# Kernel optimization log

Hardware: AMD Instinct MI355X
Metric: run time of the kernel (lower is better)

The kernel has to match this reference:

```python
import jax, jax.numpy as jnp
import numpy as np

B, S, H, I, E, K = 2, 2048, 1024, 2816, 8, 2


def setup_inputs() -> dict:
    key = jax.random.key(0)
    k1, k2, k3, k4, k5 = jax.random.split(key, 5)
    std = 0.02
    x = jax.random.normal(k1, (B, S, H), dtype=jnp.float32)
    gate_w = jax.random.normal(k2, (H, E), dtype=jnp.float32) * std   # router Linear(H,E), no bias
    Wg = jax.random.normal(k3, (E, H, I), dtype=jnp.float32) * std    # per-expert gate_proj
    Wu = jax.random.normal(k4, (E, H, I), dtype=jnp.float32) * std    # per-expert up_proj
    Wd = jax.random.normal(k5, (E, I, H), dtype=jnp.float32) * std    # per-expert down_proj
    return {"x": x, "gate_w": gate_w, "Wg": Wg, "Wu": Wu, "Wd": Wd}


def reference(x, gate_w, Wg, Wu, Wd):
    b, s, h = x.shape
    e = gate_w.shape[1]
    # --- Gating ---
    logits = jnp.einsum('bsh,he->bse', x, gate_w)                      # [B,S,E]
    top_vals, top_idx = jax.lax.top_k(logits, K)                       # [B,S,K]
    sel = (top_idx[..., None] == jnp.arange(e)).any(axis=-2)           # [B,S,E] bool, top-k mask
    sparse_logits = jnp.where(sel, logits, -jnp.inf)
    sparse_probs = jax.nn.softmax(sparse_logits, axis=-1)              # zero weight off top-k
    # --- Experts (dense over E, weighted by sparse probs; math identical to gather/scatter loop) ---
    xf = x.reshape(-1, h)                                              # [T,H], T=B*S
    g = jnp.einsum('th,ehi->tei', xf, Wg)                              # [T,E,I]
    u = jnp.einsum('th,ehi->tei', xf, Wu)
    act = jax.nn.silu(g) * u                                           # SwiGLU
    expert_out = jnp.einsum('tei,eih->teh', act, Wd)                   # [T,E,H]
    out = jnp.einsum('teh,te->th', expert_out, sparse_probs.reshape(-1, e))
    final_outputs = out.reshape(b, s, h)
    gate_logit = logits.reshape(-1, e)                                 # [B*S,E]
    return final_outputs, gate_logit
```

## Files before the change

kernel.cpp:

```cpp
#include <hip/hip_runtime.h>


namespace {
constexpr int TOKS = 4096;
constexpr int HDIM = 1024;
constexpr int IDIM = 2816;
constexpr int NEXP = 8;
constexpr int NROW = 8192;

constexpr size_t WGT_OFF = 0;
constexpr size_t WUT_OFF = 46137344;
constexpr size_t WDT_OFF = 92274688;
constexpr size_t A_OFF   = 138412032;
constexpr size_t ACT_OFF = 155189248;
constexpr size_t CNT_OFF = 201326592;
constexpr size_t OFS_OFF = CNT_OFF + 64;
constexpr size_t CUR_OFF = CNT_OFF + 128;
constexpr size_t TIX_OFF = CNT_OFF + 1024;
constexpr size_t TPR_OFF = TIX_OFF + 32768;
constexpr size_t SLT_OFF = TPR_OFF + 32768;
constexpr size_t PRT_OFF = 0;
}

typedef __attribute__((ext_vector_type(8))) short short8;
typedef __attribute__((ext_vector_type(8))) unsigned short ushort8;
typedef __attribute__((ext_vector_type(4))) float f32x4;

__device__ __forceinline__ unsigned short f2bf(float f) {
  union { float f; unsigned int u; } v; v.f = f;
  unsigned int u = v.u;
  return (unsigned short)((u + 0x7fffu + ((u >> 16) & 1u)) >> 16);
}

__device__ __forceinline__ void gl2lds16(const void* g, void* l) {
  __builtin_amdgcn_global_load_lds(
      (const __attribute__((address_space(1))) void*)g,
      (__attribute__((address_space(3))) void*)l, 16, 0, 0);
}

__global__ void k_init(int* __restrict__ cnt) {
  if (threadIdx.x < NEXP) cnt[threadIdx.x] = 0;
}

__global__ __launch_bounds__(256) void k_transpose(
    const float* __restrict__ in, unsigned short* __restrict__ out,
    int R, int C) {
  const size_t eoff = (size_t)blockIdx.z * R * C;
  in += eoff; out += eoff;
  __shared__ float tile[64][65];
  const int c0 = blockIdx.x * 64, r0 = blockIdx.y * 64;
  const int tid = threadIdx.x;
  const int rr = tid >> 4, cc4 = (tid & 15) * 4;
#pragma unroll
  for (int i = 0; i < 4; ++i) {
    int r = rr + i * 16;
    float4 v = *(const float4*)(in + (size_t)(r0 + r) * C + c0 + cc4);
    tile[r][cc4 + 0] = v.x; tile[r][cc4 + 1] = v.y;
    tile[r][cc4 + 2] = v.z; tile[r][cc4 + 3] = v.w;
  }
  __syncthreads();
  const int j = tid & 7;
#pragma unroll
  for (int i = 0; i < 2; ++i) {
    int c = (tid >> 3) + i * 32;
    ushort8 o;
#pragma unroll
    for (int k = 0; k < 8; ++k) o[k] = f2bf(tile[j * 8 + k][c]);
    *(ushort8*)(out + (size_t)(c0 + c) * R + r0 + j * 8) = o;
  }
}

__global__ __launch_bounds__(256) void k_gating(
    const float* __restrict__ x, const float* __restrict__ gw,
    float* __restrict__ logits_out, int* __restrict__ cnt,
    int2* __restrict__ tidx, float2* __restrict__ tprb) {
  const int lane = threadIdx.x & 63;
  const int t = blockIdx.x * 4 + (threadIdx.x >> 6);
  const float* xr = x + (size_t)t * HDIM;
  double acc[8];
#pragma unroll
  for (int e = 0; e < 8; ++e) acc[e] = 0.0;
#pragma unroll
  for (int j = 0; j < 16; ++j) {
    int h = lane + j * 64;
    float xv = xr[h];
    const float4* g = (const float4*)(gw + (size_t)h * 8);
    float4 g0 = g[0], g1 = g[1];
    acc[0] += (double)xv * g0.x; acc[1] += (double)xv * g0.y;
    acc[2] += (double)xv * g0.z; acc[3] += (double)xv * g0.w;
    acc[4] += (double)xv * g1.x; acc[5] += (double)xv * g1.y;
    acc[6] += (double)xv * g1.z; acc[7] += (double)xv * g1.w;
  }
#pragma unroll
  for (int off = 32; off > 0; off >>= 1) {
#pragma unroll
    for (int e = 0; e < 8; ++e) acc[e] += __shfl_down(acc[e], off);
  }
  if (lane == 0) {
    float lg[8];
#pragma unroll
    for (int e = 0; e < 8; ++e) lg[e] = (float)acc[e];
#pragma unroll
    for (int e = 0; e < 8; ++e) logits_out[(size_t)t * 8 + e] = lg[e];
    float v0 = lg[0]; int i0 = 0; float v1 = -3.0e38f; int i1 = 0;
#pragma unroll
    for (int e = 1; e < 8; ++e) {
      if (lg[e] > v0) { v1 = v0; i1 = i0; v0 = lg[e]; i0 = e; }
      else if (lg[e] > v1) { v1 = lg[e]; i1 = e; }
    }
    float ex = expf(v1 - v0);
    float p0 = 1.0f / (1.0f + ex);
    float p1 = ex / (1.0f + ex);
    tidx[t] = make_int2(i0, i1);
    tprb[t] = make_float2(p0, p1);
    atomicAdd(&cnt[i0], 1);
    atomicAdd(&cnt[i1], 1);
  }
}

__global__ void k_prefix(const int* __restrict__ cnt, int* __restrict__ offs,
                         int* __restrict__ cur) {
  if (threadIdx.x == 0) {
    int s = 0;
    for (int e = 0; e < NEXP; ++e) { offs[e] = s; cur[e] = s; s += cnt[e]; }
  }
}

__global__ __launch_bounds__(256) void k_build(
    const float* __restrict__ x, const int2* __restrict__ tidx,
    int* __restrict__ cur, int* __restrict__ slot_row,
    unsigned short* __restrict__ A) {
  const int t = blockIdx.x;
  __shared__ int rs[2];
  if (threadIdx.x == 0) {
    int2 ii = tidx[t];
    int r0 = atomicAdd(&cur[ii.x], 1);
    int r1 = atomicAdd(&cur[ii.y], 1);
    rs[0] = r0; rs[1] = r1;
    slot_row[t * 2] = r0; slot_row[t * 2 + 1] = r1;
  }
  __syncthreads();
  const int r0 = rs[0], r1 = rs[1];
  float4 v = ((const float4*)(x + (size_t)t * HDIM))[threadIdx.x];
  ushort4 b;
  b.x = f2bf(v.x); b.y = f2bf(v.y); b.z = f2bf(v.z); b.w = f2bf(v.w);
  ((ushort4*)(A + (size_t)r0 * HDIM))[threadIdx.x] = b;
  ((ushort4*)(A + (size_t)r1 * HDIM))[threadIdx.x] = b;
}

__global__ __launch_bounds__(256, 2) void k_gemm1(
    const unsigned short* __restrict__ A, const unsigned short* __restrict__ WgT,
    const unsigned short* __restrict__ WuT, unsigned short* __restrict__ act,
    const int* __restrict__ cnt, const int* __restrict__ offs) {
  const int e = blockIdx.z;
  const int ne = cnt[e];
  const int m0 = blockIdx.y * 128;
  if (m0 >= ne) return;
  const int off = offs[e];
  const int n0 = blockIdx.x * 64;
  const unsigned short* Bg = WgT + ((size_t)e * IDIM + n0) * HDIM;
  const unsigned short* Bu = WuT + ((size_t)e * IDIM + n0) * HDIM;

  __shared__ unsigned short As[128 * 64];
  __shared__ unsigned short Bgs[64 * 64];
  __shared__ unsigned short Bus[64 * 64];

  const int tid = threadIdx.x, w = tid >> 6, lane = tid & 63;
  const int lrow8 = lane >> 3;
  const int swz = ((lane & 7) ^ lrow8) * 8;
  const int m16 = lane & 15, quad = lane >> 4, l7 = lane & 7;

  f32x4 accg[2][4], accu[2][4];
#pragma unroll
  for (int mi = 0; mi < 2; ++mi)
#pragma unroll
    for (int ni = 0; ni < 4; ++ni) {
      accg[mi][ni] = (f32x4){0.f, 0.f, 0.f, 0.f};
      accu[mi][ni] = (f32x4){0.f, 0.f, 0.f, 0.f};
    }

  for (int kt = 0; kt < HDIM / 64; ++kt) {
    const int k0 = kt * 64;
#pragma unroll
    for (int i = 0; i < 4; ++i) {
      int gr = off + m0 + w * 32 + i * 8 + lrow8;
      gr = gr > (NROW - 1) ? (NROW - 1) : gr;
      gl2lds16(A + (size_t)gr * HDIM + k0 + swz, &As[(w * 32 + i * 8) * 64]);
    }
#pragma unroll
    for (int i = 0; i < 2; ++i) {
      int rl = w * 16 + i * 8 + lrow8;
      gl2lds16(Bg + (size_t)rl * HDIM + k0 + swz, &Bgs[(w * 16 + i * 8) * 64]);
      gl2lds16(Bu + (size_t)rl * HDIM + k0 + swz, &Bus[(w * 16 + i * 8) * 64]);
    }
    __syncthreads();
#pragma unroll
    for (int kk = 0; kk < 2; ++kk) {
      const int jc = ((kk * 4 + quad) ^ l7) * 8;
      short8 af[2], bgf[4], buf[4];
#pragma unroll
      for (int mi = 0; mi < 2; ++mi)
        af[mi] = *(const short8*)&As[(w * 32 + mi * 16 + m16) * 64 + jc];
#pragma unroll
      for (int ni = 0; ni < 4; ++ni) {
        bgf[ni] = *(const short8*)&Bgs[(ni * 16 + m16) * 64 + jc];
        buf[ni] = *(const short8*)&Bus[(ni * 16 + m16) * 64 + jc];
      }
#pragma unroll
      for (int mi = 0; mi < 2; ++mi)
#pragma unroll
        for (int ni = 0; ni < 4; ++ni) {
          accg[mi][ni] = __builtin_amdgcn_mfma_f32_16x16x32_bf16(
              af[mi], bgf[ni], accg[mi][ni], 0, 0, 0);
          accu[mi][ni] = __builtin_amdgcn_mfma_f32_16x16x32_bf16(
              af[mi], buf[ni], accu[mi][ni], 0, 0, 0);
        }
    }
    __syncthreads();
  }
#pragma unroll
  for (int mi = 0; mi < 2; ++mi)
#pragma unroll
    for (int ni = 0; ni < 4; ++ni)
#pragma unroll
      for (int r = 0; r < 4; ++r) {
        int ml = w * 32 + mi * 16 + quad * 4 + r;
        float g = accg[mi][ni][r];
        float u = accu[mi][ni][r];
        float s = g / (1.0f + __expf(-g));
        As[ml * 64 + ni * 16 + m16] = f2bf(s * u);
      }
  __syncthreads();
#pragma unroll
  for (int i = 0; i < 4; ++i) {
    int chunk = i * 256 + tid;
    int row = chunk >> 3, j = chunk & 7;
    if (m0 + row < ne)
      *(ushort8*)&act[(size_t)(off + m0 + row) * IDIM + n0 + j * 8] =
          *(const ushort8*)&As[row * 64 + j * 8];
  }
}

__global__ __launch_bounds__(256, 2) void k_gemm2(
    const unsigned short* __restrict__ act, const unsigned short* __restrict__ WdT,
    float* __restrict__ partial, const int* __restrict__ cnt,
    const int* __restrict__ offs) {
  const int e = blockIdx.z;
  const int ne = cnt[e];
  const int m0 = blockIdx.y * 128;
  if (m0 >= ne) return;
  const int off = offs[e];
  const int n0 = blockIdx.x * 128;
  const unsigned short* B = WdT + ((size_t)e * HDIM + n0) * IDIM;

  __shared__ unsigned short As[128 * 64];
  __shared__ unsigned short Bs[128 * 64];

  const int tid = threadIdx.x, w = tid >> 6, lane = tid & 63;
  const int lrow8 = lane >> 3;
  const int swz = ((lane & 7) ^ lrow8) * 8;
  const int m16 = lane & 15, quad = lane >> 4, l7 = lane & 7;
  const int wm = (w >> 1) * 64, wn = (w & 1) * 64;

  f32x4 acc[4][4];
#pragma unroll
  for (int mi = 0; mi < 4; ++mi)
#pragma unroll
    for (int ni = 0; ni < 4; ++ni) acc[mi][ni] = (f32x4){0.f, 0.f, 0.f, 0.f};

  for (int kt = 0; kt < IDIM / 64; ++kt) {
    const int k0 = kt * 64;
#pragma unroll
    for (int i = 0; i < 4; ++i) {
      int rl = w * 32 + i * 8 + lrow8;
      int gr = off + m0 + rl;
      gr = gr > (NROW - 1) ? (NROW - 1) : gr;
      gl2lds16(act + (size_t)gr * IDIM + k0 + swz, &As[(w * 32 + i * 8) * 64]);
      gl2lds16(B + (size_t)rl * IDIM + k0 + swz, &Bs[(w * 32 + i * 8) * 64]);
    }
    __syncthreads();
#pragma unroll
    for (int kk = 0; kk < 2; ++kk) {
      const int jc = ((kk * 4 + quad) ^ l7) * 8;
      short8 af[4], bf[4];
#pragma unroll
      for (int mi = 0; mi < 4; ++mi)
        af[mi] = *(const short8*)&As[(wm + mi * 16 + m16) * 64 + jc];
#pragma unroll
      for (int ni = 0; ni < 4; ++ni)
        bf[ni] = *(const short8*)&Bs[(wn + ni * 16 + m16) * 64 + jc];
#pragma unroll
      for (int mi = 0; mi < 4; ++mi)
#pragma unroll
        for (int ni = 0; ni < 4; ++ni)
          acc[mi][ni] = __builtin_amdgcn_mfma_f32_16x16x32_bf16(
              af[mi], bf[ni], acc[mi][ni], 0, 0, 0);
    }
    __syncthreads();
  }
#pragma unroll
  for (int mi = 0; mi < 4; ++mi)
#pragma unroll
    for (int ni = 0; ni < 4; ++ni)
#pragma unroll
      for (int r = 0; r < 4; ++r) {
        int ml = wm + mi * 16 + quad * 4 + r;
        if (m0 + ml < ne)
          partial[(size_t)(off + m0 + ml) * HDIM + n0 + wn + ni * 16 + m16] =
              acc[mi][ni][r];
      }
}

__global__ __launch_bounds__(256) void k_combine(
    const float* __restrict__ partial, const int* __restrict__ slot_row,
    const float2* __restrict__ tprb, float* __restrict__ out) {
  const int t = blockIdx.x;
  const int r0 = slot_row[2 * t], r1 = slot_row[2 * t + 1];
  const float2 p = tprb[t];
  float4 a = ((const float4*)(partial + (size_t)r0 * HDIM))[threadIdx.x];
  float4 b = ((const float4*)(partial + (size_t)r1 * HDIM))[threadIdx.x];
  float4 o;
  o.x = p.x * a.x + p.y * b.x;
  o.y = p.x * a.y + p.y * b.y;
  o.z = p.x * a.z + p.y * b.z;
  o.w = p.x * a.w + p.y * b.w;
  ((float4*)(out + (size_t)t * HDIM))[threadIdx.x] = o;
}

extern "C" void kernel_launch(void* const* d_in, const int* in_sizes, int n_in,
                              void* d_out, int out_size, void* d_ws, size_t ws_size,
                              hipStream_t stream) {
  const float* x  = (const float*)d_in[0];
  const float* gw = (const float*)d_in[1];
  const float* Wg = (const float*)d_in[2];
  const float* Wu = (const float*)d_in[3];
  const float* Wd = (const float*)d_in[4];
  float* out = (float*)d_out;
  char* ws = (char*)d_ws;

  unsigned short* WgT = (unsigned short*)(ws + WGT_OFF);
  unsigned short* WuT = (unsigned short*)(ws + WUT_OFF);
  unsigned short* WdT = (unsigned short*)(ws + WDT_OFF);
  unsigned short* A   = (unsigned short*)(ws + A_OFF);
  unsigned short* act = (unsigned short*)(ws + ACT_OFF);
  float* partial = (float*)(ws + PRT_OFF);
  int* cnt  = (int*)(ws + CNT_OFF);
  int* offs = (int*)(ws + OFS_OFF);
  int* cur  = (int*)(ws + CUR_OFF);
  int2* tidx = (int2*)(ws + TIX_OFF);
  float2* tprb = (float2*)(ws + TPR_OFF);
  int* slot_row = (int*)(ws + SLT_OFF);

  float* logits_out = out + (size_t)TOKS * HDIM;

  k_init<<<1, 64, 0, stream>>>(cnt);
  k_transpose<<<dim3(IDIM / 64, HDIM / 64, NEXP), 256, 0, stream>>>(Wg, WgT, HDIM, IDIM);
  k_transpose<<<dim3(IDIM / 64, HDIM / 64, NEXP), 256, 0, stream>>>(Wu, WuT, HDIM, IDIM);
  k_transpose<<<dim3(HDIM / 64, IDIM / 64, NEXP), 256, 0, stream>>>(Wd, WdT, IDIM, HDIM);
  k_gating<<<TOKS / 4, 256, 0, stream>>>(x, gw, logits_out, cnt, tidx, tprb);
  k_prefix<<<1, 64, 0, stream>>>(cnt, offs, cur);
  k_build<<<TOKS, 256, 0, stream>>>(x, tidx, cur, slot_row, A);
  k_gemm1<<<dim3(IDIM / 64, TOKS / 128, NEXP), 256, 0, stream>>>(A, WgT, WuT, act, cnt, offs);
  k_gemm2<<<dim3(HDIM / 128, TOKS / 128, NEXP), 256, 0, stream>>>(act, WdT, partial, cnt, offs);
  k_combine<<<TOKS, 256, 0, stream>>>(partial, slot_row, tprb, out);
}
```

Before: 710.0 us.

## Compact MoE tile list, merge transposes, and fold slot assignment into gating

Builds a compact list of (expert, row-tile) pairs in the prefix kernel so the grouped GEMMs launch only about 72 row tiles instead of 8x32 mostly-empty blocks. The three weight transposes and the counter init are merged into one launch, and per-expert slot ranks are taken from the gating atomics, which removes the second atomic pass in the build kernel. Gating also loads x with float4. This cuts launch count and wasted blocks that exit immediately, but adds a serial tile-list loop on one thread and makes the row order depend on atomic ordering.

```diff
diff --git a/kernel.cpp b/kernel.cpp
--- a/kernel.cpp
+++ b/kernel.cpp
@@ -15,10 +15,10 @@
 constexpr size_t ACT_OFF = 155189248;
 constexpr size_t CNT_OFF = 201326592;
 constexpr size_t OFS_OFF = CNT_OFF + 64;
-constexpr size_t CUR_OFF = CNT_OFF + 128;
+constexpr size_t TLN_OFF = CNT_OFF + 128;
+constexpr size_t TLS_OFF = CNT_OFF + 256;
 constexpr size_t TIX_OFF = CNT_OFF + 1024;
-constexpr size_t TPR_OFF = TIX_OFF + 32768;
-constexpr size_t SLT_OFF = TPR_OFF + 32768;
+constexpr size_t TPR_OFF = CNT_OFF + 66560;
 constexpr size_t PRT_OFF = 0;
 }
 
@@ -38,17 +38,22 @@
       (__attribute__((address_space(3))) void*)l, 16, 0, 0);
 }
 
-__global__ void k_init(int* __restrict__ cnt) {
-  if (threadIdx.x < NEXP) cnt[threadIdx.x] = 0;
-}
-
-__global__ __launch_bounds__(256) void k_transpose(
-    const float* __restrict__ in, unsigned short* __restrict__ out,
-    int R, int C) {
-  const size_t eoff = (size_t)blockIdx.z * R * C;
+__global__ __launch_bounds__(256) void k_transpose_all(
+    const float* __restrict__ Wg, const float* __restrict__ Wu,
+    const float* __restrict__ Wd, unsigned short* __restrict__ WgT,
+    unsigned short* __restrict__ WuT, unsigned short* __restrict__ WdT,
+    int* __restrict__ cnt) {
+  const int z = blockIdx.z;
+  if (z == 0 && blockIdx.x == 0 && threadIdx.x < NEXP) cnt[threadIdx.x] = 0;
+  const float* in; unsigned short* out; int C, R;
+  if (z < 8)       { in = Wg; out = WgT; C = IDIM; R = HDIM; }
+  else if (z < 16) { in = Wu; out = WuT; C = IDIM; R = HDIM; }
+  else             { in = Wd; out = WdT; C = HDIM; R = IDIM; }
+  const size_t eoff = (size_t)(z & 7) * HDIM * IDIM;
   in += eoff; out += eoff;
+  const int nbx = C / 64;
+  const int c0 = (blockIdx.x % nbx) * 64, r0 = (blockIdx.x / nbx) * 64;
   __shared__ float tile[64][65];
-  const int c0 = blockIdx.x * 64, r0 = blockIdx.y * 64;
   const int tid = threadIdx.x;
   const int rr = tid >> 4, cc4 = (tid & 15) * 4;
 #pragma unroll
@@ -73,23 +78,27 @@
 __global__ __launch_bounds__(256) void k_gating(
     const float* __restrict__ x, const float* __restrict__ gw,
     float* __restrict__ logits_out, int* __restrict__ cnt,
-    int2* __restrict__ tidx, float2* __restrict__ tprb) {
+    int4* __restrict__ tidx, float2* __restrict__ tprb) {
   const int lane = threadIdx.x & 63;
   const int t = blockIdx.x * 4 + (threadIdx.x >> 6);
-  const float* xr = x + (size_t)t * HDIM;
+  const float4* xr = (const float4*)(x + (size_t)t * HDIM);
   double acc[8];
 #pragma unroll
   for (int e = 0; e < 8; ++e) acc[e] = 0.0;
 #pragma unroll
-  for (int j = 0; j < 16; ++j) {
-    int h = lane + j * 64;
-    float xv = xr[h];
-    const float4* g = (const float4*)(gw + (size_t)h * 8);
-    float4 g0 = g[0], g1 = g[1];
-    acc[0] += (double)xv * g0.x; acc[1] += (double)xv * g0.y;
-    acc[2] += (double)xv * g0.z; acc[3] += (double)xv * g0.w;
-    acc[4] += (double)xv * g1.x; acc[5] += (double)xv * g1.y;
-    acc[6] += (double)xv * g1.z; acc[7] += (double)xv * g1.w;
+  for (int jj = 0; jj < 4; ++jj) {
+    float4 xv = xr[lane + jj * 64];
+    const int hb = (lane + jj * 64) * 4;
+    const float xs[4] = {xv.x, xv.y, xv.z, xv.w};
+#pragma unroll
+    for (int c = 0; c < 4; ++c) {
+      const float4* g = (const float4*)(gw + (size_t)(hb + c) * 8);
+      float4 g0 = g[0], g1 = g[1];
+      acc[0] += (double)xs[c] * g0.x; acc[1] += (double)xs[c] * g0.y;
+      acc[2] += (double)xs[c] * g0.z; acc[3] += (double)xs[c] * g0.w;
+      acc[4] += (double)xs[c] * g1.x; acc[5] += (double)xs[c] * g1.y;
+      acc[6] += (double)xs[c] * g1.z; acc[7] += (double)xs[c] * g1.w;
+    }
   }
 #pragma unroll
   for (int off = 32; off > 0; off >>= 1) {
@@ -111,36 +120,32 @@
     float ex = expf(v1 - v0);
     float p0 = 1.0f / (1.0f + ex);
     float p1 = ex / (1.0f + ex);
-    tidx[t] = make_int2(i0, i1);
+    int r0 = atomicAdd(&cnt[i0], 1);
+    int r1 = atomicAdd(&cnt[i1], 1);
+    tidx[t] = make_int4(i0, i1, r0, r1);
     tprb[t] = make_float2(p0, p1);
-    atomicAdd(&cnt[i0], 1);
-    atomicAdd(&cnt[i1], 1);
   }
 }
 
 __global__ void k_prefix(const int* __restrict__ cnt, int* __restrict__ offs,
-                         int* __restrict__ cur) {
+                         int2* __restrict__ tlist, int* __restrict__ tln) {
   if (threadIdx.x == 0) {
-    int s = 0;
-    for (int e = 0; e < NEXP; ++e) { offs[e] = s; cur[e] = s; s += cnt[e]; }
+    int s = 0, nt = 0;
+    for (int e = 0; e < NEXP; ++e) {
+      offs[e] = s;
+      for (int m0 = 0; m0 < cnt[e]; m0 += 128) tlist[nt++] = make_int2(e, m0);
+      s += cnt[e];
+    }
+    *tln = nt;
   }
 }
 
 __global__ __launch_bounds__(256) void k_build(
-    const float* __restrict__ x, const int2* __restrict__ tidx,
-    int* __restrict__ cur, int* __restrict__ slot_row,
-    unsigned short* __restrict__ A) {
+    const float* __restrict__ x, const int4* __restrict__ tidx,
+    const int* __restrict__ offs, unsigned short* __restrict__ A) {
   const int t = blockIdx.x;
-  __shared__ int rs[2];
-  if (threadIdx.x == 0) {
-    int2 ii = tidx[t];
-    int r0 = atomicAdd(&cur[ii.x], 1);
-    int r1 = atomicAdd(&cur[ii.y], 1);
-    rs[0] = r0; rs[1] = r1;
-    slot_row[t * 2] = r0; slot_row[t * 2 + 1] = r1;
-  }
-  __syncthreads();
-  const int r0 = rs[0], r1 = rs[1];
+  const int4 ii = tidx[t];
+  const int r0 = offs[ii.x] + ii.z, r1 = offs[ii.y] + ii.w;
   float4 v = ((const float4*)(x + (size_t)t * HDIM))[threadIdx.x];
   ushort4 b;
   b.x = f2bf(v.x); b.y = f2bf(v.y); b.z = f2bf(v.z); b.w = f2bf(v.w);
@@ -151,11 +156,12 @@
 __global__ __launch_bounds__(256, 2) void k_gemm1(
     const unsigned short* __restrict__ A, const unsigned short* __restrict__ WgT,
     const unsigned short* __restrict__ WuT, unsigned short* __restrict__ act,
-    const int* __restrict__ cnt, const int* __restrict__ offs) {
-  const int e = blockIdx.z;
+    const int* __restrict__ cnt, const int* __restrict__ offs,
+    const int2* __restrict__ tlist, const int* __restrict__ tln) {
+  if ((int)blockIdx.y >= *tln) return;
+  const int2 tl = tlist[blockIdx.y];
+  const int e = tl.x, m0 = tl.y;
   const int ne = cnt[e];
-  const int m0 = blockIdx.y * 128;
-  if (m0 >= ne) return;
   const int off = offs[e];
   const int n0 = blockIdx.x * 64;
   const unsigned short* Bg = WgT + ((size_t)e * IDIM + n0) * HDIM;
@@ -244,11 +250,12 @@
 __global__ __launch_bounds__(256, 2) void k_gemm2(
     const unsigned short* __restrict__ act, const unsigned short* __restrict__ WdT,
     float* __restrict__ partial, const int* __restrict__ cnt,
-    const int* __restrict__ offs) {
-  const int e = blockIdx.z;
+    const int* __restrict__ offs, const int2* __restrict__ tlist,
+    const int* __restrict__ tln) {
+  if ((int)blockIdx.y >= *tln) return;
+  const int2 tl = tlist[blockIdx.y];
+  const int e = tl.x, m0 = tl.y;
   const int ne = cnt[e];
-  const int m0 = blockIdx.y * 128;
-  if (m0 >= ne) return;
   const int off = offs[e];
   const int n0 = blockIdx.x * 128;
   const unsigned short* B = WdT + ((size_t)e * HDIM + n0) * IDIM;
@@ -312,10 +319,12 @@
 }
 
 __global__ __launch_bounds__(256) void k_combine(
-    const float* __restrict__ partial, const int* __restrict__ slot_row,
-    const float2* __restrict__ tprb, float* __restrict__ out) {
+    const float* __restrict__ partial, const int4* __restrict__ tidx,
+    const int* __restrict__ offs, const float2* __restrict__ tprb,
+    float* __restrict__ out) {
   const int t = blockIdx.x;
-  const int r0 = slot_row[2 * t], r1 = slot_row[2 * t + 1];
+  const int4 ii = tidx[t];
+  const int r0 = offs[ii.x] + ii.z, r1 = offs[ii.y] + ii.w;
   const float2 p = tprb[t];
   float4 a = ((const float4*)(partial + (size_t)r0 * HDIM))[threadIdx.x];
   float4 b = ((const float4*)(partial + (size_t)r1 * HDIM))[threadIdx.x];
@@ -346,21 +355,21 @@
   float* partial = (float*)(ws + PRT_OFF);
   int* cnt  = (int*)(ws + CNT_OFF);
   int* offs = (int*)(ws + OFS_OFF);
-  int* cur  = (int*)(ws + CUR_OFF);
-  int2* tidx = (int2*)(ws + TIX_OFF);
+  int* tln  = (int*)(ws + TLN_OFF);
+  int2* tlist = (int2*)(ws + TLS_OFF);
+  int4* tidx = (int4*)(ws + TIX_OFF);
   float2* tprb = (float2*)(ws + TPR_OFF);
-  int* slot_row = (int*)(ws + SLT_OFF);
 
   float* logits_out = out + (size_t)TOKS * HDIM;
 
-  k_init<<<1, 64, 0, stream>>>(cnt);
-  k_transpose<<<dim3(IDIM / 64, HDIM / 64, NEXP), 256, 0, stream>>>(Wg, WgT, HDIM, IDIM);
-  k_transpose<<<dim3(IDIM / 64, HDIM / 64, NEXP), 256, 0, stream>>>(Wu, WuT, HDIM, IDIM);
-  k_transpose<<<dim3(HDIM / 64, IDIM / 64, NEXP), 256, 0, stream>>>(Wd, WdT, IDIM, HDIM);
+  k_transpose_all<<<dim3(704, 1, 24), 256, 0, stream>>>(Wg, Wu, Wd, WgT, WuT,
+                                                        WdT, cnt);
   k_gating<<<TOKS / 4, 256, 0, stream>>>(x, gw, logits_out, cnt, tidx, tprb);
-  k_prefix<<<1, 64, 0, stream>>>(cnt, offs, cur);
-  k_build<<<TOKS, 256, 0, stream>>>(x, tidx, cur, slot_row, A);
-  k_gemm1<<<dim3(IDIM / 64, TOKS / 128, NEXP), 256, 0, stream>>>(A, WgT, WuT, act, cnt, offs);
-  k_gemm2<<<dim3(HDIM / 128, TOKS / 128, NEXP), 256, 0, stream>>>(act, WdT, partial, cnt, offs);
-  k_combine<<<TOKS, 256, 0, stream>>>(partial, slot_row, tprb, out);
-}
+  k_prefix<<<1, 64, 0, stream>>>(cnt, offs, tlist, tln);
+  k_build<<<TOKS, 256, 0, stream>>>(x, tidx, offs, A);
+  k_gemm1<<<dim3(IDIM / 64, 72), 256, 0, stream>>>(A, WgT, WuT, act, cnt, offs,
+                                                   tlist, tln);
+  k_gemm2<<<dim3(HDIM / 128, 72), 256, 0, stream>>>(act, WdT, partial, cnt,
+                                                    offs, tlist, tln);
+  k_combine<<<TOKS, 256, 0, stream>>>(partial, tidx, offs, tprb, out);
+}
```

Measured after the change: 593.0 us. -16.5%, faster.
